# Performance work log

Measured on AMD Instinct MI355X. Metric: run time of the kernel, lower is better.

## Reference

```python
import jax, jax.numpy as jnp
import numpy as np
from jax import lax

B = 128
ENC_HW = 14
IMG_DIM = 512
EMB = 512
HID = 1024
VOCAB = 10000
MAX_CAP = 20


def setup_inputs() -> dict:
    key = jax.random.key(0)
    ks = jax.random.split(key, 10)
    encoder_out = jax.random.normal(ks[0], (B, ENC_HW, ENC_HW, IMG_DIM), dtype=jnp.float32)
    encoded_captions = jax.random.randint(ks[1], (B, MAX_CAP), 0, VOCAB)
    caption_lengths = jax.random.randint(ks[2], (B, 1), 2, MAX_CAP + 1)
    caption_lengths = caption_lengths.at[0, 0].set(MAX_CAP)  # ensure max decode length is static MAX_CAP-1
    # parameters (torch-style init)
    emb_W = jax.random.uniform(ks[3], (VOCAB, EMB), minval=-0.1, maxval=0.1, dtype=jnp.float32)
    kimg = 1.0 / np.sqrt(IMG_DIM * ENC_HW * ENC_HW)
    img_W = jax.random.uniform(ks[4], (EMB, IMG_DIM * ENC_HW * ENC_HW), minval=-kimg, maxval=kimg, dtype=jnp.float32)
    img_b = jnp.zeros((EMB,), jnp.float32)
    kl = 1.0 / np.sqrt(HID)
    W_ih = jax.random.uniform(ks[5], (4 * HID, EMB), minval=-kl, maxval=kl, dtype=jnp.float32)
    W_hh = jax.random.uniform(ks[6], (4 * HID, HID), minval=-kl, maxval=kl, dtype=jnp.float32)
    b_ih = jax.random.uniform(ks[7], (4 * HID,), minval=-kl, maxval=kl, dtype=jnp.float32)
    b_hh = jax.random.uniform(ks[8], (4 * HID,), minval=-kl, maxval=kl, dtype=jnp.float32)
    fc_W = jax.random.uniform(ks[9], (VOCAB, HID), minval=-0.1, maxval=0.1, dtype=jnp.float32)
    fc_b = jnp.zeros((VOCAB,), jnp.float32)
    return {
        "encoder_out": encoder_out,
        "encoded_captions": encoded_captions,
        "caption_lengths": caption_lengths,
        "emb_W": emb_W, "img_W": img_W, "img_b": img_b,
        "W_ih": W_ih, "W_hh": W_hh, "b_ih": b_ih, "b_hh": b_hh,
        "fc_W": fc_W, "fc_b": fc_b,
    }


def reference(encoder_out, encoded_captions, caption_lengths,
              emb_W, img_W, img_b, W_ih, W_hh, b_ih, b_hh, fc_W, fc_b):
    b = encoder_out.shape[0]
    lens = caption_lengths[:, 0]
    sort_ind = jnp.argsort(-lens, stable=True)          # descending sort of lengths
    lens_s = lens[sort_ind]
    enc = encoder_out.reshape(b, -1)[sort_ind]          # [B, img_dim*hw*hw]
    caps = encoded_captions[sort_ind]                   # [B, MAX_CAP]
    x_img = enc @ img_W.T + img_b                       # [B, EMB]
    emb = emb_W[caps]                                   # [B, MAX_CAP, EMB]
    dec_len = lens_s - 1                                # decode lengths
    T = caps.shape[1] - 1                               # static max decode length

    h0 = jnp.zeros((b, W_hh.shape[1]), encoder_out.dtype)
    c0 = jnp.zeros_like(h0)

    def step(carry, t):
        h, c = carry
        # t==0 uses the encoded image, afterwards embeddings[:, t-1]
        x_t = jnp.where(t == 0, x_img,
                        jnp.take(emb, jnp.maximum(t - 1, 0), axis=1))
        gates = x_t @ W_ih.T + b_ih + h @ W_hh.T + b_hh  # [B, 4H]
        i, f, g, o = jnp.split(gates, 4, axis=1)
        i = jax.nn.sigmoid(i); f = jax.nn.sigmoid(f)
        g = jnp.tanh(g);       o = jax.nn.sigmoid(o)
        c_new = f * c + i * g
        h_new = o * jnp.tanh(c_new)
        active = (dec_len >= t)[:, None]                 # rows still decoding (l > t-1)
        h = jnp.where(active, h_new, h)
        c = jnp.where(active, c_new, c)
        # dropout is identity in eval mode (deterministic reference)
        preds = jnp.where(active, h_new @ fc_W.T + fc_b, 0.0)
        return (h, c), preds

    (_, _), preds = lax.scan(step, (h0, c0), jnp.arange(T))
    predictions = jnp.transpose(preds, (1, 0, 2))        # [B, T, VOCAB]
    return predictions, caps, dec_len, sort_ind
```

## Files before the change

kernel.cpp:

```cpp
#include <hip/hip_runtime.h>

#define BB 128
#define TT 19
#define MAXCAP 20
#define EMBD 512
#define HIDD 1024
#define NVOCAB 10000
#define KIMG 100352
#define NGATE 4096

#define FC_NT 79
#define FC_BLOCKS (FC_NT*2)
#define LSTM_BLOCKS 128
#define COMBO_BLOCKS (FC_BLOCKS + LSTM_BLOCKS)

typedef unsigned short u16;
typedef unsigned int   u32;
using bfrag = __attribute__((ext_vector_type(8))) short;
using ff4   = __attribute__((ext_vector_type(4))) float;
static_assert(sizeof(bfrag) == 16, "bfrag must be 16B");
static_assert(sizeof(ff4) == 16, "ff4 must be 16B");

__device__ __forceinline__ void bsplit(float x, u16 &h, u16 &l) {
    u32 u = __float_as_uint(x);
    h = (u16)(u >> 16);
    float hf = __uint_as_float(u & 0xffff0000u);
    l = (u16)(__float_as_uint(x - hf) >> 16);
}


__global__ void prep_kernel(const int* __restrict__ cap_len,
                            const int* __restrict__ caps,
                            int* __restrict__ sort_ind,
                            int* __restrict__ dec_len,
                            int* __restrict__ nAct,
                            int* __restrict__ caps_s,
                            float* __restrict__ out_tail)
{
    __shared__ int lens[BB];
    __shared__ int sind[BB];
    __shared__ int sdl[BB];
    int i = threadIdx.x;
    lens[i] = cap_len[i];
    __syncthreads();
    int li = lens[i];
    int r = 0;
    for (int j = 0; j < BB; ++j) {
        int lj = lens[j];
        r += (lj > li) | ((lj == li) & (j < i));
    }
    sind[r] = i;
    __syncthreads();
    int src = sind[i];
    sort_ind[i] = src;
    int dl = lens[src] - 1;
    dec_len[i] = dl;
    sdl[i] = dl;
    for (int tt2 = 0; tt2 < MAXCAP; ++tt2) {
        int v = caps[src*MAXCAP + tt2];
        caps_s[i*MAXCAP + tt2] = v;
        out_tail[i*MAXCAP + tt2] = (float)v;
    }
    out_tail[BB*MAXCAP + i] = (float)dl;
    out_tail[BB*MAXCAP + BB + i] = (float)src;
    __syncthreads();
    if (i < 20) {
        int cnt = 0;
        for (int j = 0; j < BB; ++j) cnt += (sdl[j] >= i);
        nAct[i] = cnt;
    }
}

__global__ void init_kernel(float* __restrict__ x_img,
                            const float* __restrict__ img_b,
                            float* __restrict__ h2,
                            float* __restrict__ c2)
{
    int idx = blockIdx.x*blockDim.x + threadIdx.x;
    int stride = gridDim.x*blockDim.x;
    for (int i = idx; i < BB*EMBD; i += stride) x_img[i] = img_b[i & (EMBD-1)];
    for (int i = idx; i < 2*BB*HIDD; i += stride) { h2[i] = 0.f; c2[i] = 0.f; }
}

__global__ __launch_bounds__(256) void fcw_conv(const float* __restrict__ fcW,
                                                u16* __restrict__ hi,
                                                u16* __restrict__ lo)
{
    size_t i = ((size_t)blockIdx.x*256 + threadIdx.x)*8;
    float4 f0 = *(const float4*)(fcW + i);
    float4 f1 = *(const float4*)(fcW + i + 4);
    float v[8] = {f0.x,f0.y,f0.z,f0.w,f1.x,f1.y,f1.z,f1.w};
    u32 hp[4], lp[4];
    #pragma unroll
    for (int j = 0; j < 4; ++j) {
        u16 h0,l0,h1,l1;
        bsplit(v[2*j],   h0, l0);
        bsplit(v[2*j+1], h1, l1);
        hp[j] = (u32)h0 | ((u32)h1 << 16);
        lp[j] = (u32)l0 | ((u32)l1 << 16);
    }
    *(uint4*)(hi + i) = make_uint4(hp[0],hp[1],hp[2],hp[3]);
    *(uint4*)(lo + i) = make_uint4(lp[0],lp[1],lp[2],lp[3]);
}

__global__ __launch_bounds__(256) void img_gemm(const float* __restrict__ enc,
                                                const float* __restrict__ img_W,
                                                const int* __restrict__ sort_ind,
                                                float* __restrict__ x_img)
{
    __shared__ float As[32][68];
    __shared__ float Bs[32][132];
    __shared__ int rows[64];
    const int nt = blockIdx.x;
    const int mt = blockIdx.y & 1;
    const int ks = blockIdx.y >> 1;
    const int m0 = mt*64, n0 = nt*128;
    const int k0 = ks * (KIMG/32);
    const int tid = threadIdx.x;
    if (tid < 64) rows[tid] = sort_ind[m0 + tid];
    __syncthreads();
    const int kq = tid & 7;
    const int rr = tid >> 3;
    const int tx = tid & 15, ty = tid >> 4;
    float acc[4][8] = {{0.f}};
    const float* a0p = enc   + (size_t)rows[rr]      * KIMG + k0 + kq*4;
    const float* a1p = enc   + (size_t)rows[rr+32]   * KIMG + k0 + kq*4;
    const float* b0p = img_W + (size_t)(n0+rr)       * KIMG + k0 + kq*4;
    const float* b1p = img_W + (size_t)(n0+rr+32)    * KIMG + k0 + kq*4;
    const float* b2p = img_W + (size_t)(n0+rr+64)    * KIMG + k0 + kq*4;
    const float* b3p = img_W + (size_t)(n0+rr+96)    * KIMG + k0 + kq*4;
    for (int kb = 0; kb < 98; ++kb) {
        float4 a0 = *(const float4*)(a0p + kb*32);
        float4 a1 = *(const float4*)(a1p + kb*32);
        float4 b0 = *(const float4*)(b0p + kb*32);
        float4 b1 = *(const float4*)(b1p + kb*32);
        float4 b2 = *(const float4*)(b2p + kb*32);
        float4 b3 = *(const float4*)(b3p + kb*32);
        __syncthreads();
        As[kq*4+0][rr]    = a0.x; As[kq*4+1][rr]    = a0.y; As[kq*4+2][rr]    = a0.z; As[kq*4+3][rr]    = a0.w;
        As[kq*4+0][rr+32] = a1.x; As[kq*4+1][rr+32] = a1.y; As[kq*4+2][rr+32] = a1.z; As[kq*4+3][rr+32] = a1.w;
        Bs[kq*4+0][rr]    = b0.x; Bs[kq*4+1][rr]    = b0.y; Bs[kq*4+2][rr]    = b0.z; Bs[kq*4+3][rr]    = b0.w;
        Bs[kq*4+0][rr+32] = b1.x; Bs[kq*4+1][rr+32] = b1.y; Bs[kq*4+2][rr+32] = b1.z; Bs[kq*4+3][rr+32] = b1.w;
        Bs[kq*4+0][rr+64] = b2.x; Bs[kq*4+1][rr+64] = b2.y; Bs[kq*4+2][rr+64] = b2.z; Bs[kq*4+3][rr+64] = b2.w;
        Bs[kq*4+0][rr+96] = b3.x; Bs[kq*4+1][rr+96] = b3.y; Bs[kq*4+2][rr+96] = b3.z; Bs[kq*4+3][rr+96] = b3.w;
        __syncthreads();
        #pragma unroll
        for (int kk = 0; kk < 32; ++kk) {
            float4 av  = *(const float4*)&As[kk][ty*4];
            float4 blo = *(const float4*)&Bs[kk][tx*4];
            float4 bhi = *(const float4*)&Bs[kk][64 + tx*4];
            float aa[4] = {av.x,av.y,av.z,av.w};
            float bb[8] = {blo.x,blo.y,blo.z,blo.w,bhi.x,bhi.y,bhi.z,bhi.w};
            #pragma unroll
            for (int i2 = 0; i2 < 4; ++i2)
                #pragma unroll
                for (int j2 = 0; j2 < 8; ++j2)
                    acc[i2][j2] = fmaf(aa[i2], bb[j2], acc[i2][j2]);
        }
    }
    #pragma unroll
    for (int i2 = 0; i2 < 4; ++i2) {
        int m = m0 + ty*4 + i2;
        #pragma unroll
        for (int j2 = 0; j2 < 4; ++j2)
            atomicAdd(&x_img[m*EMBD + n0 + tx*4 + j2],      acc[i2][j2]);
        #pragma unroll
        for (int j2 = 0; j2 < 4; ++j2)
            atomicAdd(&x_img[m*EMBD + n0 + 64 + tx*4 + j2], acc[i2][4+j2]);
    }
}

__global__ __launch_bounds__(256) void xg_gemm(int tBase,
    const float* __restrict__ x_img, const float* __restrict__ emb_W,
    const int* __restrict__ caps_s,
    const float* __restrict__ W_ih,
    const float* __restrict__ b_ih, const float* __restrict__ b_hh,
    float* __restrict__ xgOut)
{
    __shared__ float As[32][132];
    __shared__ float Bs[32][68];
    __shared__ const float* Arow[128];
    const int t  = tBase + blockIdx.y;
    const int n0 = blockIdx.x * 64;
    const int tid = threadIdx.x;
    if (tid < 128) {
        Arow[tid] = (t == 0) ? (x_img + tid*EMBD)
                             : (emb_W + (size_t)caps_s[tid*MAXCAP + (t-1)]*EMBD);
    }
    __syncthreads();
    const int kq = tid & 7, rr = tid >> 3;
    const int tx = tid & 15, ty = tid >> 4;
    float acc[8][4] = {{0.f}};
    for (int kb = 0; kb < 16; ++kb) {
        const int k = kb*32 + kq*4;
        float4 a[4];
        #pragma unroll
        for (int rd = 0; rd < 4; ++rd)
            a[rd] = *(const float4*)(Arow[rd*32 + rr] + k);
        float4 b0 = *(const float4*)&W_ih[(size_t)(n0+rr)   *EMBD + k];
        float4 b1 = *(const float4*)&W_ih[(size_t)(n0+rr+32)*EMBD + k];
        __syncthreads();
        #pragma unroll
        for (int rd = 0; rd < 4; ++rd) {
            As[kq*4+0][rd*32+rr] = a[rd].x; As[kq*4+1][rd*32+rr] = a[rd].y;
            As[kq*4+2][rd*32+rr] = a[rd].z; As[kq*4+3][rd*32+rr] = a[rd].w;
        }
        Bs[kq*4+0][rr]    = b0.x; Bs[kq*4+1][rr]    = b0.y; Bs[kq*4+2][rr]    = b0.z; Bs[kq*4+3][rr]    = b0.w;
        Bs[kq*4+0][rr+32] = b1.x; Bs[kq*4+1][rr+32] = b1.y; Bs[kq*4+2][rr+32] = b1.z; Bs[kq*4+3][rr+32] = b1.w;
        __syncthreads();
        #pragma unroll
        for (int kk = 0; kk < 32; ++kk) {
            float4 alo = *(const float4*)&As[kk][ty*4];
            float4 ahi = *(const float4*)&As[kk][64 + ty*4];
            float4 bv  = *(const float4*)&Bs[kk][tx*4];
            float aa[8] = {alo.x,alo.y,alo.z,alo.w,ahi.x,ahi.y,ahi.z,ahi.w};
            float bb[4] = {bv.x,bv.y,bv.z,bv.w};
            #pragma unroll
            for (int i2 = 0; i2 < 8; ++i2)
                #pragma unroll
                for (int j2 = 0; j2 < 4; ++j2)
                    acc[i2][j2] = fmaf(aa[i2], bb[j2], acc[i2][j2]);
        }
    }
    #pragma unroll
    for (int i2 = 0; i2 < 8; ++i2) {
        int m = (i2 < 4) ? (ty*4 + i2) : (64 + ty*4 + (i2-4));
        #pragma unroll
        for (int j2 = 0; j2 < 4; ++j2) {
            int n = n0 + tx*4 + j2;
            xgOut[((size_t)blockIdx.y*BB + m)*NGATE + n] = acc[i2][j2] + b_ih[n] + b_hh[n];
        }
    }
}

__global__ __launch_bounds__(256) void combo_kernel(int t,
    float* __restrict__ h2, float* __restrict__ c2,
    const float* __restrict__ W_hh,
    const float* __restrict__ xgt,
    const float* __restrict__ fc_W, const float* __restrict__ fc_b,
    const int* __restrict__ nAct,
    float* __restrict__ out,
    u16* __restrict__ h_hi2, u16* __restrict__ h_lo2,
    const u16* __restrict__ fcw_hi, const u16* __restrict__ fcw_lo,
    int preconv)
{
    __shared__ __align__(16) float smem[32*68 + 32*132];
    const int tid = threadIdx.x;
    const int bid = blockIdx.x;

    if (bid < FC_BLOCKS) {
        if (t == 0) return;
        const int nA = nAct[t-1];
        const int nt0 = bid % FC_NT, mt = bid / FC_NT;
        const int m0 = mt*64, n0 = nt0*128;
        if (m0 >= nA) return;
        u16* H = (u16*)smem;
        u16* L = H + 128*40;
        const int lane = tid & 63, w = tid >> 6;
        const int lr = lane & 15, lk = lane >> 4;
        const u16* pAh = h_hi2 + (size_t)(t & 1)*BB*HIDD + (size_t)(m0 + w*16 + lr)*HIDD;
        const u16* pAl = h_lo2 + (size_t)(t & 1)*BB*HIDD + (size_t)(m0 + w*16 + lr)*HIDD;
        const int row = tid >> 1, half = tid & 1;
        const int gn = n0 + row;
        const bool gv = gn < NVOCAB;
        ff4 acc[8];
        #pragma unroll
        for (int i = 0; i < 8; ++i) acc[i] = (ff4){0.f,0.f,0.f,0.f};

        for (int ks = 0; ks < 32; ++ks) {
            const int k0 = ks*32;
            __syncthreads();
            const int dst = row*40 + half*16;
            if (preconv) {
                uint4 z = make_uint4(0,0,0,0);
                const uint4* ph = (const uint4*)(fcw_hi + (size_t)gn*HIDD + k0 + half*16);
                const uint4* pl = (const uint4*)(fcw_lo + (size_t)gn*HIDD + k0 + half*16);
                uint4 h0 = gv ? ph[0] : z, h1 = gv ? ph[1] : z;
                uint4 l0 = gv ? pl[0] : z, l1 = gv ? pl[1] : z;
                *(uint4*)&H[dst]   = h0;  *(uint4*)&H[dst+8] = h1;
                *(uint4*)&L[dst]   = l0;  *(uint4*)&L[dst+8] = l1;
            } else {
                float v[16];
                const float4* pf = (const float4*)(fc_W + (size_t)gn*HIDD + k0 + half*16);
                #pragma unroll
                for (int q = 0; q < 4; ++q) {
                    float4 f = gv ? pf[q] : make_float4(0.f,0.f,0.f,0.f);
                    v[q*4+0]=f.x; v[q*4+1]=f.y; v[q*4+2]=f.z; v[q*4+3]=f.w;
                }
                u32 hp[8], lp[8];
                #pragma unroll
                for (int q = 0; q < 8; ++q) {
                    u16 h0,l0,h1,l1;
                    bsplit(v[2*q],h0,l0); bsplit(v[2*q+1],h1,l1);
                    hp[q] = (u32)h0 | ((u32)h1<<16);
                    lp[q] = (u32)l0 | ((u32)l1<<16);
                }
                *(uint4*)&H[dst]   = make_uint4(hp[0],hp[1],hp[2],hp[3]);
                *(uint4*)&H[dst+8] = make_uint4(hp[4],hp[5],hp[6],hp[7]);
                *(uint4*)&L[dst]   = make_uint4(lp[0],lp[1],lp[2],lp[3]);
                *(uint4*)&L[dst+8] = make_uint4(lp[4],lp[5],lp[6],lp[7]);
            }
            __syncthreads();
            bfrag a_h = *(const bfrag*)(pAh + k0 + lk*8);
            bfrag a_l = *(const bfrag*)(pAl + k0 + lk*8);
            #pragma unroll
            for (int nt = 0; nt < 8; ++nt) {
                const int br = (nt*16 + lr)*40 + lk*8;
                bfrag b_h = *(const bfrag*)&H[br];
                bfrag b_l = *(const bfrag*)&L[br];
                acc[nt] = __builtin_amdgcn_mfma_f32_16x16x32_bf16(a_h, b_h, acc[nt], 0,0,0);
                acc[nt] = __builtin_amdgcn_mfma_f32_16x16x32_bf16(a_h, b_l, acc[nt], 0,0,0);
                acc[nt] = __builtin_amdgcn_mfma_f32_16x16x32_bf16(a_l, b_h, acc[nt], 0,0,0);
            }
        }
        #pragma unroll
        for (int nt = 0; nt < 8; ++nt) {
            const int n = n0 + nt*16 + lr;
            if (n >= NVOCAB) continue;
            const float bias = fc_b[n];
            #pragma unroll
            for (int r = 0; r < 4; ++r) {
                const int m = m0 + w*16 + lk*4 + r;
                if (m < nA)
                    out[(size_t)m*(TT*NVOCAB) + (size_t)(t-1)*NVOCAB + n] = acc[nt][r] + bias;
            }
        }
    } else {
        if (t > TT-1) return;
        const int nA = nAct[t];
        const int lb = bid - FC_BLOCKS;
        const int jt = lb & 31, mt2 = lb >> 5;
        const int j0 = jt*32, m0 = mt2*32;
        if (m0 >= nA) return;
        float (*As)[36]   = (float (*)[36])smem;
        float (*BsL)[132] = (float (*)[132])(smem + 32*36);
        const float* hr  = h2 + (size_t)(t & 1)*BB*HIDD;
        float*       hw  = h2 + (size_t)((t+1) & 1)*BB*HIDD;
        const float* cr  = c2 + (size_t)(t & 1)*BB*HIDD;
        float*       cw  = c2 + (size_t)((t+1) & 1)*BB*HIDD;
        u16* hwh = h_hi2 + (size_t)((t+1) & 1)*BB*HIDD;
        u16* hwl = h_lo2 + (size_t)((t+1) & 1)*BB*HIDD;
        const int kq = tid & 7, rr = tid >> 3;
        const int tx = tid & 31, ty = tid >> 5;
        float acc[4][4] = {{0.f}};
        for (int kb = 0; kb < 32; ++kb) {
            const int k = kb*32 + kq*4;
            float4 a = *(const float4*)&hr[(size_t)(m0+rr)*HIDD + k];
            float4 b[4];
            #pragma unroll
            for (int s = 0; s < 4; ++s)
                b[s] = *(const float4*)&W_hh[(size_t)(s*HIDD + j0 + rr)*HIDD + k];
            __syncthreads();
            As[kq*4+0][rr] = a.x; As[kq*4+1][rr] = a.y; As[kq*4+2][rr] = a.z; As[kq*4+3][rr] = a.w;
            #pragma unroll
            for (int s = 0; s < 4; ++s) {
                BsL[kq*4+0][s*33+rr] = b[s].x; BsL[kq*4+1][s*33+rr] = b[s].y;
                BsL[kq*4+2][s*33+rr] = b[s].z; BsL[kq*4+3][s*33+rr] = b[s].w;
            }
            __syncthreads();
            #pragma unroll
            for (int kk = 0; kk < 32; ++kk) {
                float4 av = *(const float4*)&As[kk][ty*4];
                float aa[4] = {av.x, av.y, av.z, av.w};
                float bb[4] = {BsL[kk][0*33+tx], BsL[kk][1*33+tx],
                               BsL[kk][2*33+tx], BsL[kk][3*33+tx]};
                #pragma unroll
                for (int s = 0; s < 4; ++s)
                    #pragma unroll
                    for (int r2 = 0; r2 < 4; ++r2)
                        acc[s][r2] = fmaf(aa[r2], bb[s], acc[s][r2]);
            }
        }
        const int j = j0 + tx;
        #pragma unroll
        for (int r2 = 0; r2 < 4; ++r2) {
            const int m = m0 + ty*4 + r2;
            if (m >= nA) continue;
            const float iv = acc[0][r2] + xgt[(size_t)m*NGATE + j];
            const float fv = acc[1][r2] + xgt[(size_t)m*NGATE + HIDD + j];
            const float gv = acc[2][r2] + xgt[(size_t)m*NGATE + 2*HIDD + j];
            const float ov = acc[3][r2] + xgt[(size_t)m*NGATE + 3*HIDD + j];
            const float ig = 1.f/(1.f + expf(-iv));
            const float fg = 1.f/(1.f + expf(-fv));
            const float gg = tanhf(gv);
            const float og = 1.f/(1.f + expf(-ov));
            const float cn = fg*cr[(size_t)m*HIDD + j] + ig*gg;
            const float hn = og*tanhf(cn);
            cw[(size_t)m*HIDD + j] = cn;
            hw[(size_t)m*HIDD + j] = hn;
            u16 sh, sl; bsplit(hn, sh, sl);
            hwh[(size_t)m*HIDD + j] = sh;
            hwl[(size_t)m*HIDD + j] = sl;
        }
    }
}

extern "C" void kernel_launch(void* const* d_in, const int* in_sizes, int n_in,
                              void* d_out, int out_size, void* d_ws, size_t ws_size,
                              hipStream_t stream)
{
    const float* enc   = (const float*)d_in[0];
    const int*   caps  = (const int*)d_in[1];
    const int*   clen  = (const int*)d_in[2];
    const float* emb_W = (const float*)d_in[3];
    const float* img_W = (const float*)d_in[4];
    const float* img_b = (const float*)d_in[5];
    const float* W_ih  = (const float*)d_in[6];
    const float* W_hh  = (const float*)d_in[7];
    const float* b_ih  = (const float*)d_in[8];
    const float* b_hh  = (const float*)d_in[9];
    const float* fc_W  = (const float*)d_in[10];
    const float* fc_b  = (const float*)d_in[11];
    float* out = (float*)d_out;

    int* sort_ind = (int*)d_ws;
    int* dec_len  = sort_ind + BB;
    int* nAct     = dec_len + BB;
    int* caps_s   = nAct + 24;
    float* x_img  = (float*)(caps_s + BB*MAXCAP);
    float* h2     = x_img + BB*EMBD;
    float* c2     = h2 + 2*BB*HIDD;
    u16*   h_hi2  = (u16*)(c2 + 2*BB*HIDD);
    u16*   h_lo2  = h_hi2 + 2*BB*HIDD;
    float* xg     = (float*)(h_lo2 + 2*BB*HIDD);
    u16*   fcw_hi = (u16*)(xg + (size_t)TT*BB*NGATE);
    u16*   fcw_lo = fcw_hi + (size_t)NVOCAB*HIDD;

    const size_t min_end = (size_t)((char*)(xg + (size_t)BB*NGATE) - (char*)d_ws);
    const size_t xg_end  = (size_t)((char*)fcw_hi - (char*)d_ws);
    const size_t all_end = (size_t)((char*)(fcw_lo + (size_t)NVOCAB*HIDD) - (char*)d_ws);
    const bool ws_ok   = ws_size >= min_end;
    const bool full    = ws_size >= xg_end;
    const bool preconv = ws_size >= all_end;

    hipMemsetAsync(out, 0, (size_t)BB*TT*NVOCAB*sizeof(float), stream);
    if (!ws_ok) return;

    float* out_tail = out + (size_t)BB*TT*NVOCAB;

    hipLaunchKernelGGL(prep_kernel, dim3(1), dim3(BB), 0, stream,
                       clen, caps, sort_ind, dec_len, nAct, caps_s, out_tail);
    hipLaunchKernelGGL(init_kernel, dim3(512), dim3(256), 0, stream,
                       x_img, img_b, h2, c2);
    if (preconv) {
        hipLaunchKernelGGL(fcw_conv, dim3(5000), dim3(256), 0, stream,
                           fc_W, fcw_hi, fcw_lo);
    }
    hipLaunchKernelGGL(img_gemm, dim3(4, 64), dim3(256), 0, stream,
                       enc, img_W, sort_ind, x_img);
    if (full) {
        hipLaunchKernelGGL(xg_gemm, dim3(64, TT), dim3(256), 0, stream,
                           0, x_img, emb_W, caps_s, W_ih, b_ih, b_hh, xg);
    }
    for (int t = 0; t <= TT; ++t) {
        if (!full && t < TT) {
            hipLaunchKernelGGL(xg_gemm, dim3(64, 1), dim3(256), 0, stream,
                               t, x_img, emb_W, caps_s, W_ih, b_ih, b_hh, xg);
        }
        const float* xgt = full ? (xg + (size_t)(t < TT ? t : 0)*BB*NGATE) : xg;
        hipLaunchKernelGGL(combo_kernel, dim3(COMBO_BLOCKS), dim3(256), 0, stream,
                           t, h2, c2, W_hh, xgt, fc_W, fc_b, nAct, out,
                           h_hi2, h_lo2, fcw_hi, fcw_lo, (int)preconv);
    }
}
```

Measured before the change: 2.229 ms.

## Defer vocab projection to one batched MFMA GEMM after LSTM recurrence

Splits the fused per-step LSTM/FC kernel into two parts. A lighter per-step LSTM kernel uses 16-row tiles and register prefetch of the next K slice, and stores bf16 hi/lo hidden states for every timestep. A single fc_gemm_all kernel then handles two timesteps per block, so each staged fc_W tile is reused across both steps. img_gemm also moves to a finer split-K grid with register double-buffering. Together these aim to cut repeated fc_W streaming and per-step launch and serialization cost, at the price of a larger hidden-state workspace.

```diff
diff --git a/kernel.cpp b/kernel.cpp
--- a/kernel.cpp
+++ b/kernel.cpp
@@ -9,11 +9,6 @@
 #define KIMG 100352
 #define NGATE 4096
 
-#define FC_NT 79
-#define FC_BLOCKS (FC_NT*2)
-#define LSTM_BLOCKS 128
-#define COMBO_BLOCKS (FC_BLOCKS + LSTM_BLOCKS)
-
 typedef unsigned short u16;
 typedef unsigned int   u32;
 using bfrag = __attribute__((ext_vector_type(8))) short;
@@ -27,7 +22,6 @@
     float hf = __uint_as_float(u & 0xffff0000u);
     l = (u16)(__float_as_uint(x - hf) >> 16);
 }
-
 
 __global__ void prep_kernel(const int* __restrict__ cap_len,
                             const int* __restrict__ caps,
@@ -115,7 +109,7 @@
     const int mt = blockIdx.y & 1;
     const int ks = blockIdx.y >> 1;
     const int m0 = mt*64, n0 = nt*128;
-    const int k0 = ks * (KIMG/32);
+    const int k0 = ks * 1024;
     const int tid = threadIdx.x;
     if (tid < 64) rows[tid] = sort_ind[m0 + tid];
     __syncthreads();
@@ -129,21 +123,30 @@
     const float* b1p = img_W + (size_t)(n0+rr+32)    * KIMG + k0 + kq*4;
     const float* b2p = img_W + (size_t)(n0+rr+64)    * KIMG + k0 + kq*4;
     const float* b3p = img_W + (size_t)(n0+rr+96)    * KIMG + k0 + kq*4;
-    for (int kb = 0; kb < 98; ++kb) {
-        float4 a0 = *(const float4*)(a0p + kb*32);
-        float4 a1 = *(const float4*)(a1p + kb*32);
-        float4 b0 = *(const float4*)(b0p + kb*32);
-        float4 b1 = *(const float4*)(b1p + kb*32);
-        float4 b2 = *(const float4*)(b2p + kb*32);
-        float4 b3 = *(const float4*)(b3p + kb*32);
-        __syncthreads();
-        As[kq*4+0][rr]    = a0.x; As[kq*4+1][rr]    = a0.y; As[kq*4+2][rr]    = a0.z; As[kq*4+3][rr]    = a0.w;
-        As[kq*4+0][rr+32] = a1.x; As[kq*4+1][rr+32] = a1.y; As[kq*4+2][rr+32] = a1.z; As[kq*4+3][rr+32] = a1.w;
-        Bs[kq*4+0][rr]    = b0.x; Bs[kq*4+1][rr]    = b0.y; Bs[kq*4+2][rr]    = b0.z; Bs[kq*4+3][rr]    = b0.w;
-        Bs[kq*4+0][rr+32] = b1.x; Bs[kq*4+1][rr+32] = b1.y; Bs[kq*4+2][rr+32] = b1.z; Bs[kq*4+3][rr+32] = b1.w;
-        Bs[kq*4+0][rr+64] = b2.x; Bs[kq*4+1][rr+64] = b2.y; Bs[kq*4+2][rr+64] = b2.z; Bs[kq*4+3][rr+64] = b2.w;
-        Bs[kq*4+0][rr+96] = b3.x; Bs[kq*4+1][rr+96] = b3.y; Bs[kq*4+2][rr+96] = b3.z; Bs[kq*4+3][rr+96] = b3.w;
-        __syncthreads();
+    float4 a0c = *(const float4*)a0p;
+    float4 a1c = *(const float4*)a1p;
+    float4 b0c = *(const float4*)b0p;
+    float4 b1c = *(const float4*)b1p;
+    float4 b2c = *(const float4*)b2p;
+    float4 b3c = *(const float4*)b3p;
+    for (int kb = 0; kb < 32; ++kb) {
+        __syncthreads();
+        As[kq*4+0][rr]    = a0c.x; As[kq*4+1][rr]    = a0c.y; As[kq*4+2][rr]    = a0c.z; As[kq*4+3][rr]    = a0c.w;
+        As[kq*4+0][rr+32] = a1c.x; As[kq*4+1][rr+32] = a1c.y; As[kq*4+2][rr+32] = a1c.z; As[kq*4+3][rr+32] = a1c.w;
+        Bs[kq*4+0][rr]    = b0c.x; Bs[kq*4+1][rr]    = b0c.y; Bs[kq*4+2][rr]    = b0c.z; Bs[kq*4+3][rr]    = b0c.w;
+        Bs[kq*4+0][rr+32] = b1c.x; Bs[kq*4+1][rr+32] = b1c.y; Bs[kq*4+2][rr+32] = b1c.z; Bs[kq*4+3][rr+32] = b1c.w;
+        Bs[kq*4+0][rr+64] = b2c.x; Bs[kq*4+1][rr+64] = b2c.y; Bs[kq*4+2][rr+64] = b2c.z; Bs[kq*4+3][rr+64] = b2c.w;
+        Bs[kq*4+0][rr+96] = b3c.x; Bs[kq*4+1][rr+96] = b3c.y; Bs[kq*4+2][rr+96] = b3c.z; Bs[kq*4+3][rr+96] = b3c.w;
+        __syncthreads();
+        if (kb < 31) {
+            const int off = (kb+1)*32;
+            a0c = *(const float4*)(a0p + off);
+            a1c = *(const float4*)(a1p + off);
+            b0c = *(const float4*)(b0p + off);
+            b1c = *(const float4*)(b1p + off);
+            b2c = *(const float4*)(b2p + off);
+            b3c = *(const float4*)(b3p + off);
+        }
         #pragma unroll
         for (int kk = 0; kk < 32; ++kk) {
             float4 av  = *(const float4*)&As[kk][ty*4];
@@ -233,164 +236,182 @@
     }
 }
 
-__global__ __launch_bounds__(256) void combo_kernel(int t,
+__global__ __launch_bounds__(256) void lstm_step(int t,
     float* __restrict__ h2, float* __restrict__ c2,
-    const float* __restrict__ W_hh,
-    const float* __restrict__ xgt,
-    const float* __restrict__ fc_W, const float* __restrict__ fc_b,
+    const float* __restrict__ W_hh, const float* __restrict__ xgt,
     const int* __restrict__ nAct,
-    float* __restrict__ out,
-    u16* __restrict__ h_hi2, u16* __restrict__ h_lo2,
-    const u16* __restrict__ fcw_hi, const u16* __restrict__ fcw_lo,
-    int preconv)
-{
-    __shared__ __align__(16) float smem[32*68 + 32*132];
+    u16* __restrict__ hseq_hi, u16* __restrict__ hseq_lo)
+{
+    __shared__ float As[32][36];
+    __shared__ float BsL[32][132];
     const int tid = threadIdx.x;
-    const int bid = blockIdx.x;
-
-    if (bid < FC_BLOCKS) {
-        if (t == 0) return;
-        const int nA = nAct[t-1];
-        const int nt0 = bid % FC_NT, mt = bid / FC_NT;
-        const int m0 = mt*64, n0 = nt0*128;
-        if (m0 >= nA) return;
-        u16* H = (u16*)smem;
-        u16* L = H + 128*40;
-        const int lane = tid & 63, w = tid >> 6;
-        const int lr = lane & 15, lk = lane >> 4;
-        const u16* pAh = h_hi2 + (size_t)(t & 1)*BB*HIDD + (size_t)(m0 + w*16 + lr)*HIDD;
-        const u16* pAl = h_lo2 + (size_t)(t & 1)*BB*HIDD + (size_t)(m0 + w*16 + lr)*HIDD;
-        const int row = tid >> 1, half = tid & 1;
-        const int gn = n0 + row;
-        const bool gv = gn < NVOCAB;
-        ff4 acc[8];
-        #pragma unroll
-        for (int i = 0; i < 8; ++i) acc[i] = (ff4){0.f,0.f,0.f,0.f};
-
-        for (int ks = 0; ks < 32; ++ks) {
-            const int k0 = ks*32;
-            __syncthreads();
-            const int dst = row*40 + half*16;
-            if (preconv) {
-                uint4 z = make_uint4(0,0,0,0);
-                const uint4* ph = (const uint4*)(fcw_hi + (size_t)gn*HIDD + k0 + half*16);
-                const uint4* pl = (const uint4*)(fcw_lo + (size_t)gn*HIDD + k0 + half*16);
-                uint4 h0 = gv ? ph[0] : z, h1 = gv ? ph[1] : z;
-                uint4 l0 = gv ? pl[0] : z, l1 = gv ? pl[1] : z;
-                *(uint4*)&H[dst]   = h0;  *(uint4*)&H[dst+8] = h1;
-                *(uint4*)&L[dst]   = l0;  *(uint4*)&L[dst+8] = l1;
-            } else {
-                float v[16];
-                const float4* pf = (const float4*)(fc_W + (size_t)gn*HIDD + k0 + half*16);
-                #pragma unroll
-                for (int q = 0; q < 4; ++q) {
-                    float4 f = gv ? pf[q] : make_float4(0.f,0.f,0.f,0.f);
-                    v[q*4+0]=f.x; v[q*4+1]=f.y; v[q*4+2]=f.z; v[q*4+3]=f.w;
-                }
-                u32 hp[8], lp[8];
-                #pragma unroll
-                for (int q = 0; q < 8; ++q) {
-                    u16 h0,l0,h1,l1;
-                    bsplit(v[2*q],h0,l0); bsplit(v[2*q+1],h1,l1);
-                    hp[q] = (u32)h0 | ((u32)h1<<16);
-                    lp[q] = (u32)l0 | ((u32)l1<<16);
-                }
-                *(uint4*)&H[dst]   = make_uint4(hp[0],hp[1],hp[2],hp[3]);
-                *(uint4*)&H[dst+8] = make_uint4(hp[4],hp[5],hp[6],hp[7]);
-                *(uint4*)&L[dst]   = make_uint4(lp[0],lp[1],lp[2],lp[3]);
-                *(uint4*)&L[dst+8] = make_uint4(lp[4],lp[5],lp[6],lp[7]);
-            }
-            __syncthreads();
-            bfrag a_h = *(const bfrag*)(pAh + k0 + lk*8);
-            bfrag a_l = *(const bfrag*)(pAl + k0 + lk*8);
-            #pragma unroll
-            for (int nt = 0; nt < 8; ++nt) {
-                const int br = (nt*16 + lr)*40 + lk*8;
-                bfrag b_h = *(const bfrag*)&H[br];
-                bfrag b_l = *(const bfrag*)&L[br];
-                acc[nt] = __builtin_amdgcn_mfma_f32_16x16x32_bf16(a_h, b_h, acc[nt], 0,0,0);
-                acc[nt] = __builtin_amdgcn_mfma_f32_16x16x32_bf16(a_h, b_l, acc[nt], 0,0,0);
-                acc[nt] = __builtin_amdgcn_mfma_f32_16x16x32_bf16(a_l, b_h, acc[nt], 0,0,0);
-            }
-        }
-        #pragma unroll
-        for (int nt = 0; nt < 8; ++nt) {
-            const int n = n0 + nt*16 + lr;
-            if (n >= NVOCAB) continue;
-            const float bias = fc_b[n];
-            #pragma unroll
-            for (int r = 0; r < 4; ++r) {
-                const int m = m0 + w*16 + lk*4 + r;
-                if (m < nA)
-                    out[(size_t)m*(TT*NVOCAB) + (size_t)(t-1)*NVOCAB + n] = acc[nt][r] + bias;
-            }
-        }
-    } else {
-        if (t > TT-1) return;
-        const int nA = nAct[t];
-        const int lb = bid - FC_BLOCKS;
-        const int jt = lb & 31, mt2 = lb >> 5;
-        const int j0 = jt*32, m0 = mt2*32;
-        if (m0 >= nA) return;
-        float (*As)[36]   = (float (*)[36])smem;
-        float (*BsL)[132] = (float (*)[132])(smem + 32*36);
-        const float* hr  = h2 + (size_t)(t & 1)*BB*HIDD;
-        float*       hw  = h2 + (size_t)((t+1) & 1)*BB*HIDD;
-        const float* cr  = c2 + (size_t)(t & 1)*BB*HIDD;
-        float*       cw  = c2 + (size_t)((t+1) & 1)*BB*HIDD;
-        u16* hwh = h_hi2 + (size_t)((t+1) & 1)*BB*HIDD;
-        u16* hwl = h_lo2 + (size_t)((t+1) & 1)*BB*HIDD;
-        const int kq = tid & 7, rr = tid >> 3;
-        const int tx = tid & 31, ty = tid >> 5;
-        float acc[4][4] = {{0.f}};
-        for (int kb = 0; kb < 32; ++kb) {
-            const int k = kb*32 + kq*4;
-            float4 a = *(const float4*)&hr[(size_t)(m0+rr)*HIDD + k];
-            float4 b[4];
+    const int nA = nAct[t];
+    const int jt = blockIdx.x & 31, mt = blockIdx.x >> 5;
+    const int j0 = jt*32, m0 = mt*16;
+    if (m0 >= nA) return;
+    const float* hr = h2 + (size_t)(t & 1)*BB*HIDD;
+    float*       hw = h2 + (size_t)((t+1) & 1)*BB*HIDD;
+    const float* cr = c2 + (size_t)(t & 1)*BB*HIDD;
+    float*       cw = c2 + (size_t)((t+1) & 1)*BB*HIDD;
+    const int kq = tid & 7, rr = tid >> 3;
+    const int tx = tid & 31, ty = tid >> 5;
+    const float* aBase = hr + (size_t)(m0 + (rr & 15))*HIDD;
+    float4 a_cur = *(const float4*)(aBase + kq*4);
+    float4 b_cur[4];
+    #pragma unroll
+    for (int s = 0; s < 4; ++s)
+        b_cur[s] = *(const float4*)&W_hh[(size_t)(s*HIDD + j0 + rr)*HIDD + kq*4];
+    float acc[4][2] = {{0.f}};
+    for (int kb = 0; kb < 32; ++kb) {
+        __syncthreads();
+        if (rr < 16) {
+            As[kq*4+0][rr] = a_cur.x; As[kq*4+1][rr] = a_cur.y;
+            As[kq*4+2][rr] = a_cur.z; As[kq*4+3][rr] = a_cur.w;
+        }
+        #pragma unroll
+        for (int s = 0; s < 4; ++s) {
+            BsL[kq*4+0][s*33+rr] = b_cur[s].x; BsL[kq*4+1][s*33+rr] = b_cur[s].y;
+            BsL[kq*4+2][s*33+rr] = b_cur[s].z; BsL[kq*4+3][s*33+rr] = b_cur[s].w;
+        }
+        __syncthreads();
+        if (kb < 31) {
+            const int k = (kb+1)*32 + kq*4;
+            a_cur = *(const float4*)(aBase + k);
             #pragma unroll
             for (int s = 0; s < 4; ++s)
-                b[s] = *(const float4*)&W_hh[(size_t)(s*HIDD + j0 + rr)*HIDD + k];
-            __syncthreads();
-            As[kq*4+0][rr] = a.x; As[kq*4+1][rr] = a.y; As[kq*4+2][rr] = a.z; As[kq*4+3][rr] = a.w;
+                b_cur[s] = *(const float4*)&W_hh[(size_t)(s*HIDD + j0 + rr)*HIDD + k];
+        }
+        #pragma unroll
+        for (int kk = 0; kk < 32; ++kk) {
+            float2 av = *(const float2*)&As[kk][ty*2];
+            float aa[2] = {av.x, av.y};
+            float bb[4] = {BsL[kk][0*33+tx], BsL[kk][1*33+tx],
+                           BsL[kk][2*33+tx], BsL[kk][3*33+tx]};
             #pragma unroll
-            for (int s = 0; s < 4; ++s) {
-                BsL[kq*4+0][s*33+rr] = b[s].x; BsL[kq*4+1][s*33+rr] = b[s].y;
-                BsL[kq*4+2][s*33+rr] = b[s].z; BsL[kq*4+3][s*33+rr] = b[s].w;
+            for (int s = 0; s < 4; ++s)
+                #pragma unroll
+                for (int r2 = 0; r2 < 2; ++r2)
+                    acc[s][r2] = fmaf(aa[r2], bb[s], acc[s][r2]);
+        }
+    }
+    const int j = j0 + tx;
+    #pragma unroll
+    for (int r2 = 0; r2 < 2; ++r2) {
+        const int m = m0 + ty*2 + r2;
+        if (m >= nA) continue;
+        const float iv = acc[0][r2] + xgt[(size_t)m*NGATE + j];
+        const float fv = acc[1][r2] + xgt[(size_t)m*NGATE + HIDD + j];
+        const float gv = acc[2][r2] + xgt[(size_t)m*NGATE + 2*HIDD + j];
+        const float ov = acc[3][r2] + xgt[(size_t)m*NGATE + 3*HIDD + j];
+        const float ig = 1.f/(1.f + expf(-iv));
+        const float fg = 1.f/(1.f + expf(-fv));
+        const float gg = tanhf(gv);
+        const float og = 1.f/(1.f + expf(-ov));
+        const float cn = fg*cr[(size_t)m*HIDD + j] + ig*gg;
+        const float hn = og*tanhf(cn);
+        cw[(size_t)m*HIDD + j] = cn;
+        hw[(size_t)m*HIDD + j] = hn;
+        u16 sh, sl; bsplit(hn, sh, sl);
+        hseq_hi[((size_t)t*BB + m)*HIDD + j] = sh;
+        hseq_lo[((size_t)t*BB + m)*HIDD + j] = sl;
+    }
+}
+
+__global__ __launch_bounds__(512) void fc_gemm_all(
+    const u16* __restrict__ hseq_hi, const u16* __restrict__ hseq_lo,
+    const float* __restrict__ fc_W,
+    const u16* __restrict__ fcw_hi, const u16* __restrict__ fcw_lo,
+    const float* __restrict__ fc_b, const int* __restrict__ nAct,
+    float* __restrict__ out, int preconv)
+{
+    __shared__ __align__(16) u16 H[128*40];
+    __shared__ __align__(16) u16 L[128*40];
+    const int tid = threadIdx.x;
+    const int n0 = blockIdx.x * 128;
+    const int t0 = blockIdx.y * 2;
+    const int t1 = t0 + 1;
+    const int lane = tid & 63, w = tid >> 6;
+    const int lr = lane & 15, lk = lane >> 4;
+    const int nA0 = nAct[t0];
+    const int nA1 = (t1 < TT) ? nAct[t1] : 0;
+    const bool act0 = (w*16) < nA0;
+    const bool act1 = (w*16) < nA1;
+    const int row = tid >> 2, q = tid & 3;
+    const int gn = n0 + row;
+    const bool gv = gn < NVOCAB;
+    const int t1c = (t1 < TT) ? t1 : 0;
+    const u16* pA0h = hseq_hi + ((size_t)t0*BB  + w*16 + lr)*HIDD;
+    const u16* pA0l = hseq_lo + ((size_t)t0*BB  + w*16 + lr)*HIDD;
+    const u16* pA1h = hseq_hi + ((size_t)t1c*BB + w*16 + lr)*HIDD;
+    const u16* pA1l = hseq_lo + ((size_t)t1c*BB + w*16 + lr)*HIDD;
+    ff4 acc0[8], acc1[8];
+    #pragma unroll
+    for (int i = 0; i < 8; ++i) { acc0[i] = (ff4){0.f,0.f,0.f,0.f}; acc1[i] = (ff4){0.f,0.f,0.f,0.f}; }
+
+    auto loadStage = [&](int kbase, uint4 &hp, uint4 &lp) {
+        const uint4 z = make_uint4(0,0,0,0);
+        if (preconv) {
+            hp = gv ? *(const uint4*)(fcw_hi + (size_t)gn*HIDD + kbase + q*8) : z;
+            lp = gv ? *(const uint4*)(fcw_lo + (size_t)gn*HIDD + kbase + q*8) : z;
+        } else {
+            float4 f0 = gv ? *(const float4*)(fc_W + (size_t)gn*HIDD + kbase + q*8)     : make_float4(0,0,0,0);
+            float4 f1 = gv ? *(const float4*)(fc_W + (size_t)gn*HIDD + kbase + q*8 + 4) : make_float4(0,0,0,0);
+            float v[8] = {f0.x,f0.y,f0.z,f0.w,f1.x,f1.y,f1.z,f1.w};
+            u32 hpw[4], lpw[4];
+            #pragma unroll
+            for (int j2 = 0; j2 < 4; ++j2) {
+                u16 h0,l0,h1,l1;
+                bsplit(v[2*j2],h0,l0); bsplit(v[2*j2+1],h1,l1);
+                hpw[j2] = (u32)h0 | ((u32)h1<<16);
+                lpw[j2] = (u32)l0 | ((u32)l1<<16);
             }
-            __syncthreads();
-            #pragma unroll
-            for (int kk = 0; kk < 32; ++kk) {
-                float4 av = *(const float4*)&As[kk][ty*4];
-                float aa[4] = {av.x, av.y, av.z, av.w};
-                float bb[4] = {BsL[kk][0*33+tx], BsL[kk][1*33+tx],
-                               BsL[kk][2*33+tx], BsL[kk][3*33+tx]};
-                #pragma unroll
-                for (int s = 0; s < 4; ++s)
-                    #pragma unroll
-                    for (int r2 = 0; r2 < 4; ++r2)
-                        acc[s][r2] = fmaf(aa[r2], bb[s], acc[s][r2]);
+            hp = make_uint4(hpw[0],hpw[1],hpw[2],hpw[3]);
+            lp = make_uint4(lpw[0],lpw[1],lpw[2],lpw[3]);
+        }
+    };
+
+    uint4 hp_cur, lp_cur;
+    loadStage(0, hp_cur, lp_cur);
+    for (int ks = 0; ks < 32; ++ks) {
+        const int k0 = ks*32;
+        __syncthreads();
+        *(uint4*)&H[row*40 + q*8] = hp_cur;
+        *(uint4*)&L[row*40 + q*8] = lp_cur;
+        __syncthreads();
+        if (ks < 31) loadStage(k0 + 32, hp_cur, lp_cur);
+        bfrag a0h = *(const bfrag*)(pA0h + k0 + lk*8);
+        bfrag a0l = *(const bfrag*)(pA0l + k0 + lk*8);
+        bfrag a1h = *(const bfrag*)(pA1h + k0 + lk*8);
+        bfrag a1l = *(const bfrag*)(pA1l + k0 + lk*8);
+        #pragma unroll
+        for (int nt = 0; nt < 8; ++nt) {
+            const int br = (nt*16 + lr)*40 + lk*8;
+            bfrag bh = *(const bfrag*)&H[br];
+            bfrag bl = *(const bfrag*)&L[br];
+            if (act0) {
+                acc0[nt] = __builtin_amdgcn_mfma_f32_16x16x32_bf16(a0h, bh, acc0[nt], 0,0,0);
+                acc0[nt] = __builtin_amdgcn_mfma_f32_16x16x32_bf16(a0h, bl, acc0[nt], 0,0,0);
+                acc0[nt] = __builtin_amdgcn_mfma_f32_16x16x32_bf16(a0l, bh, acc0[nt], 0,0,0);
             }
-        }
-        const int j = j0 + tx;
-        #pragma unroll
-        for (int r2 = 0; r2 < 4; ++r2) {
-            const int m = m0 + ty*4 + r2;
-            if (m >= nA) continue;
-            const float iv = acc[0][r2] + xgt[(size_t)m*NGATE + j];
-            const float fv = acc[1][r2] + xgt[(size_t)m*NGATE + HIDD + j];
-            const float gv = acc[2][r2] + xgt[(size_t)m*NGATE + 2*HIDD + j];
-            const float ov = acc[3][r2] + xgt[(size_t)m*NGATE + 3*HIDD + j];
-            const float ig = 1.f/(1.f + expf(-iv));
-            const float fg = 1.f/(1.f + expf(-fv));
-            const float gg = tanhf(gv);
-            const float og = 1.f/(1.f + expf(-ov));
-            const float cn = fg*cr[(size_t)m*HIDD + j] + ig*gg;
-            const float hn = og*tanhf(cn);
-            cw[(size_t)m*HIDD + j] = cn;
-            hw[(size_t)m*HIDD + j] = hn;
-            u16 sh, sl; bsplit(hn, sh, sl);
-            hwh[(size_t)m*HIDD + j] = sh;
-            hwl[(size_t)m*HIDD + j] = sl;
+            if (act1) {
+                acc1[nt] = __builtin_amdgcn_mfma_f32_16x16x32_bf16(a1h, bh, acc1[nt], 0,0,0);
+                acc1[nt] = __builtin_amdgcn_mfma_f32_16x16x32_bf16(a1h, bl, acc1[nt], 0,0,0);
+                acc1[nt] = __builtin_amdgcn_mfma_f32_16x16x32_bf16(a1l, bh, acc1[nt], 0,0,0);
+            }
+        }
+    }
+    #pragma unroll
+    for (int nt = 0; nt < 8; ++nt) {
+        const int n = n0 + nt*16 + lr;
+        if (n >= NVOCAB) continue;
+        const float bias = fc_b[n];
+        #pragma unroll
+        for (int r = 0; r < 4; ++r) {
+            const int mloc = w*16 + lk*4 + r;
+            if (mloc < nA0)
+                out[(size_t)mloc*(TT*NVOCAB) + (size_t)t0*NVOCAB + n] = acc0[nt][r] + bias;
+            if (mloc < nA1)
+                out[(size_t)mloc*(TT*NVOCAB) + (size_t)t1*NVOCAB + n] = acc1[nt][r] + bias;
         }
     }
 }
@@ -420,11 +441,11 @@
     float* x_img  = (float*)(caps_s + BB*MAXCAP);
     float* h2     = x_img + BB*EMBD;
     float* c2     = h2 + 2*BB*HIDD;
-    u16*   h_hi2  = (u16*)(c2 + 2*BB*HIDD);
-    u16*   h_lo2  = h_hi2 + 2*BB*HIDD;
-    float* xg     = (float*)(h_lo2 + 2*BB*HIDD);
-    u16*   fcw_hi = (u16*)(xg + (size_t)TT*BB*NGATE);
-    u16*   fcw_lo = fcw_hi + (size_t)NVOCAB*HIDD;
+    u16* hseq_hi  = (u16*)(c2 + 2*BB*HIDD);
+    u16* hseq_lo  = hseq_hi + (size_t)TT*BB*HIDD;
+    float* xg     = (float*)(hseq_lo + (size_t)TT*BB*HIDD);
+    u16* fcw_hi   = (u16*)(xg + (size_t)TT*BB*NGATE);
+    u16* fcw_lo   = fcw_hi + (size_t)NVOCAB*HIDD;
 
     const size_t min_end = (size_t)((char*)(xg + (size_t)BB*NGATE) - (char*)d_ws);
     const size_t xg_end  = (size_t)((char*)fcw_hi - (char*)d_ws);
@@ -446,20 +467,21 @@
         hipLaunchKernelGGL(fcw_conv, dim3(5000), dim3(256), 0, stream,
                            fc_W, fcw_hi, fcw_lo);
     }
-    hipLaunchKernelGGL(img_gemm, dim3(4, 64), dim3(256), 0, stream,
+    hipLaunchKernelGGL(img_gemm, dim3(4, 196), dim3(256), 0, stream,
                        enc, img_W, sort_ind, x_img);
     if (full) {
         hipLaunchKernelGGL(xg_gemm, dim3(64, TT), dim3(256), 0, stream,
                            0, x_img, emb_W, caps_s, W_ih, b_ih, b_hh, xg);
     }
-    for (int t = 0; t <= TT; ++t) {
-        if (!full && t < TT) {
+    for (int t = 0; t < TT; ++t) {
+        if (!full) {
             hipLaunchKernelGGL(xg_gemm, dim3(64, 1), dim3(256), 0, stream,
                                t, x_img, emb_W, caps_s, W_ih, b_ih, b_hh, xg);
         }
-        const float* xgt = full ? (xg + (size_t)(t < TT ? t : 0)*BB*NGATE) : xg;
-        hipLaunchKernelGGL(combo_kernel, dim3(COMBO_BLOCKS), dim3(256), 0, stream,
-                           t, h2, c2, W_hh, xgt, fc_W, fc_b, nAct, out,
-                           h_hi2, h_lo2, fcw_hi, fcw_lo, (int)preconv);
-    }
-}
+        const float* xgt = full ? (xg + (size_t)t*BB*NGATE) : xg;
+        hipLaunchKernelGGL(lstm_step, dim3(256), dim3(256), 0, stream,
+                           t, h2, c2, W_hh, xgt, nAct, hseq_hi, hseq_lo);
+    }
+    hipLaunchKernelGGL(fc_gemm_all, dim3(79, 10), dim3(512), 0, stream,
+                       hseq_hi, hseq_lo, fc_W, fcw_hi, fcw_lo, fc_b, nAct, out, (int)preconv);
+}
```

Result: no change. 2.260 ms (+1.4%).
